# Kernel optimization log

Measured on AMD Instinct MI355X. Metric: run time of the kernel, lower is better.

## Reference

```python
import math
import jax, jax.numpy as jnp
import numpy as np

NH, HD, CHUNK, PAST, FUT = 12, 128, 128, 127, 0  # heads, head_dim, chunk, left-1, right
CTX = CHUNK + PAST + FUT                          # 255
Q_SCALE = HD ** (-0.5) / math.log(2.0)
K_SCALE = math.log1p(math.e) / math.log(2.0)
SOFTCAP = 50.0


def setup_inputs() -> dict:
    key = jax.random.key(0)
    ks = jax.random.split(key, 8)
    B, S, H = 4, 4096, NH * HD
    return {
        "hidden_states": jax.random.normal(ks[0], (B, S, H), jnp.float32),
        "position_embeddings": jax.random.normal(ks[1], (CTX, H), jnp.float32),
        "Wq": jax.random.normal(ks[2], (H, H), jnp.float32) * 0.02,
        "Wk": jax.random.normal(ks[3], (H, H), jnp.float32) * 0.02,
        "Wv": jax.random.normal(ks[4], (H, H), jnp.float32) * 0.02,
        "Wrel": jax.random.normal(ks[5], (H, H), jnp.float32) * 0.02,
        "Wpost": jax.random.normal(ks[6], (H, H), jnp.float32) * 0.02,
        "per_dim_scale": jax.random.normal(ks[7], (HD,), jnp.float32) * 0.1,
    }


def reference(hidden_states, position_embeddings, Wq, Wk, Wv, Wrel, Wpost, per_dim_scale):
    B, S, H = hidden_states.shape
    # projections -> [B, S, nh, hd]; per-dim softplus scaling on queries (Gemma audio)
    q = (hidden_states @ Wq.T).reshape(B, S, NH, HD)
    q = q * (Q_SCALE * jax.nn.softplus(per_dim_scale))
    k = (hidden_states @ Wk.T).reshape(B, S, NH, HD) * K_SCALE
    v = (hidden_states @ Wv.T).reshape(B, S, NH, HD)

    NB = (S + CHUNK - 1) // CHUNK
    pad = NB * CHUNK - S
    q_blk = jnp.pad(q, ((0, 0), (0, pad), (0, 0), (0, 0))).reshape(B, NB, CHUNK, NH, HD)

    def extract_block_context(x):
        # pad [PAST] front, [FUT + CHUNK - 1] back; overlapping windows of CTX, stride CHUNK
        xp = jnp.pad(x, ((0, 0), (PAST, FUT + CHUNK - 1), (0, 0), (0, 0)))
        idx = jnp.arange(NB)[:, None] * CHUNK + jnp.arange(CTX)[None, :]  # [NB, CTX]
        return xp[:, idx]  # [B, NB, CTX, nh, hd]

    k_ctx = extract_block_context(k)
    v_ctx = extract_block_context(v)

    # content scores: [B, nh, NB, CHUNK, CTX]
    ac = jnp.einsum('bnchd,bnxhd->bhncx', q_blk, k_ctx)

    # relative-position scores with Transformer-XL style rel_shift
    rel_k = (position_embeddings @ Wrel.T).reshape(-1, NH, HD)  # [P, nh, hd]
    bd = jnp.einsum('bnchd,phd->bhncp', q_blk, rel_k)            # [B, nh, NB, CHUNK, P]
    P = bd.shape[-1]
    bd = jnp.pad(bd, ((0, 0), (0, 0), (0, 0), (0, 0), (0, CTX + 1 - P)))
    bd = bd.reshape(B, NH, NB, CHUNK * (CTX + 1))[..., : CHUNK * CTX]
    bd = bd.reshape(B, NH, NB, CHUNK, CTX)

    logits = SOFTCAP * jnp.tanh((ac + bd) / SOFTCAP)  # softcap
    w = jax.nn.softmax(logits, axis=-1)

    out = jnp.einsum('bhncx,bnxhd->bnchd', w, v_ctx)  # [B, NB, CHUNK, nh, hd]
    out = out.reshape(B, NB * CHUNK, NH * HD)[:, :S]
    return out @ Wpost.T
```

## Files before the change

kernel.cpp:

```cpp
#include <hip/hip_runtime.h>
#include <hip/hip_bf16.h>
#include <math.h>


#define NH_    12
#define HD_    128
#define H_     1536
#define B_     4
#define S_     4096
#define CHUNK_ 128
#define CTX_   255
#define NB_CH  32
#define QKW_   3072
#define BSTR_  4352

typedef unsigned short u16;
typedef short bf16x8 __attribute__((ext_vector_type(8)));
typedef float f32x4 __attribute__((ext_vector_type(4)));

static constexpr float Q_SCALE_F = (float)(0.08838834764831845 / 0.6931471805599453);
static constexpr float K_SCALE_F = (float)(1.3132616875182228 / 0.6931471805599453);

__device__ __forceinline__ u16 f2bf(float f) {
    __hip_bfloat16 h = __float2bfloat16(f);
    return __builtin_bit_cast(u16, h);
}
__device__ __forceinline__ float bf2f(u16 u) {
    unsigned int t = ((unsigned int)u) << 16;
    return __builtin_bit_cast(float, t);
}
__device__ __forceinline__ float fast_tanh(float t) {
    float u = __expf(-2.f * fabsf(t));
    float r = (1.f - u) / (1.f + u);
    return (t < 0.f) ? -r : r;
}

__device__ __forceinline__ void gload_lds16(const u16* src_global, u16* dst_lds) {
    __builtin_amdgcn_global_load_lds(
        (const __attribute__((address_space(1))) unsigned int*)src_global,
        (__attribute__((address_space(3))) unsigned int*)dst_lds,
        16, 0, 0);
}

__global__ __launch_bounds__(256)
void conv_bf16(const float* __restrict__ src, long long base,
               u16* __restrict__ dst, long long n,
               long long zero_below, long long zero_from,
               int mode, const float* __restrict__ pds, int ncols)
{
    long long i = ((long long)blockIdx.x * 256 + threadIdx.x) * 4;
    if (i >= n) return;
    float4 v = make_float4(0.f, 0.f, 0.f, 0.f);
    if (i >= zero_below && i < zero_from)
        v = *(const float4*)(src + base + i);
    float s = 1.f;
    if (mode == 1) {
        int row = (int)(i / ncols);
        float x = pds[row & 127];
        float sp = (x > 20.f) ? x : log1pf(__expf(x));
        s = Q_SCALE_F * sp;
    } else if (mode == 2) {
        s = K_SCALE_F;
    }
    ushort4 o = make_ushort4(f2bf(v.x * s), f2bf(v.y * s), f2bf(v.z * s), f2bf(v.w * s));
    *(ushort4*)(dst + i) = o;
}

__global__ __launch_bounds__(256)
void conv_hs(const float* __restrict__ src, long long src_row0,
             u16* __restrict__ dst, long long nelem)
{
    long long i = ((long long)blockIdx.x * 256 + threadIdx.x) * 4;
    if (i >= nelem) return;
    const int row = (int)(i / H_);
    const int col = (int)(i - (long long)row * H_);
    const int b = row / BSTR_;
    const int local = row - b * BSTR_;
    float4 v = make_float4(0.f, 0.f, 0.f, 0.f);
    if (local >= 128 && local < 128 + S_) {
        const long long srow = src_row0 + (long long)b * S_ + local - 128;
        v = *(const float4*)(src + srow * H_ + col);
    }
    ushort4 o = make_ushort4(f2bf(v.x), f2bf(v.y), f2bf(v.z), f2bf(v.w));
    *(ushort4*)(dst + i) = o;
}

#define STAGE(kt, bufc) do {                                                   \
    const int _ko = (kt) << 5;                                                 \
    gload_lds16(srcA[0] + _ko, lds + (bufc) * 4096 + pbase[0]);                \
    gload_lds16(srcA[1] + _ko, lds + (bufc) * 4096 + pbase[1]);                \
    gload_lds16(srcB[0] + _ko, lds + 16384 + (bufc) * 4096 + pbase[0]);        \
    gload_lds16(srcB[1] + _ko, lds + 16384 + (bufc) * 4096 + pbase[1]);        \
} while (0)

#define READF(afX, bfX, b) do {                                                \
    _Pragma("unroll")                                                          \
    for (int m = 0; m < 4; ++m)                                                \
        afX[m] = *(const bf16x8*)&lds[(b) * 4096 + (wr + m * 16 + lr) * 32 + sw8]; \
    _Pragma("unroll")                                                          \
    for (int n = 0; n < 4; ++n)                                                \
        bfX[n] = *(const bf16x8*)&lds[16384 + (b) * 4096 + (wc + n * 16 + lr) * 32 + sw8]; \
} while (0)

#define MFMA16(afX, bfX) do {                                                  \
    __builtin_amdgcn_s_setprio(1);                                             \
    _Pragma("unroll")                                                          \
    for (int m = 0; m < 4; ++m)                                                \
        _Pragma("unroll")                                                      \
        for (int n = 0; n < 4; ++n)                                            \
            acc[m][n] = __builtin_amdgcn_mfma_f32_16x16x32_bf16(afX[m], bfX[n], acc[m][n], 0, 0, 0); \
    __builtin_amdgcn_s_setprio(0);                                             \
} while (0)

#define ITER(t, b, afC, bfC, afN, bfN) do {                                    \
    if ((t) + 2 < nk) {                                                        \
        STAGE((t) + 2, ((b) + 2) & 3);                                         \
        asm volatile("s_waitcnt vmcnt(4)" ::: "memory");                       \
    } else {                                                                   \
        asm volatile("s_waitcnt vmcnt(0)" ::: "memory");                       \
    }                                                                          \
    __builtin_amdgcn_s_barrier();                                              \
    if ((t) + 1 < nk) READF(afN, bfN, ((b) + 1) & 3);                          \
    MFMA16(afC, bfC);                                                          \
} while (0)

__global__ __launch_bounds__(256)
void gemm_bt(const u16* __restrict__ A, const u16* __restrict__ B,
             u16* __restrict__ Cp, int M, int N, int K, int ldc)
{
    __shared__ __align__(16) u16 lds[32768];

    const int tid = threadIdx.x;
    const int w = tid >> 6, l = tid & 63;
    const int lr = l & 15, lg = l >> 4;
    const int bm = blockIdx.y * 128, bn = blockIdx.x * 128;
    const int wr = (w >> 1) * 64, wc = (w & 1) * 64;
    const int sw8 = (lg ^ ((lr >> 1) & 3)) * 8;

    const u16* srcA[2];
    const u16* srcB[2];
    int pbase[2];
#pragma unroll
    for (int c = 0; c < 2; ++c) {
        const int p = (w * 2 + c) * 64 + l;
        const int row = p >> 2;
        const int s_log = (p & 3) ^ ((row >> 1) & 3);
        pbase[c] = p * 8;
        srcA[c] = A + (size_t)(bm + row) * K + s_log * 8;
        srcB[c] = B + (size_t)(bn + row) * K + s_log * 8;
    }

    f32x4 acc[4][4];
#pragma unroll
    for (int m = 0; m < 4; ++m)
#pragma unroll
        for (int n = 0; n < 4; ++n) acc[m][n] = (f32x4){0.f, 0.f, 0.f, 0.f};

    const int nk = K >> 5;
    bf16x8 af0[4], bf0[4], af1[4], bf1[4];

    STAGE(0, 0);
    STAGE(1, 1);
    asm volatile("s_waitcnt vmcnt(4)" ::: "memory");
    __builtin_amdgcn_s_barrier();
    READF(af0, bf0, 0);

    for (int t0 = 0; t0 < nk; t0 += 4) {
        ITER(t0 + 0, 0, af0, bf0, af1, bf1);
        ITER(t0 + 1, 1, af1, bf1, af0, bf0);
        ITER(t0 + 2, 2, af0, bf0, af1, bf1);
        ITER(t0 + 3, 3, af1, bf1, af0, bf0);
    }

#pragma unroll
    for (int h = 0; h < 2; ++h) {
        if (wr == h * 64) {
#pragma unroll
            for (int m = 0; m < 4; ++m)
#pragma unroll
                for (int n = 0; n < 4; ++n)
#pragma unroll
                    for (int r = 0; r < 4; ++r)
                        lds[(m * 16 + lg * 4 + r) * 136 + wc + n * 16 + lr] =
                            f2bf(acc[m][n][r]);
        }
        __syncthreads();
#pragma unroll
        for (int it = 0; it < 4; ++it) {
            const int sid = it * 256 + tid;
            const int row = sid >> 4, sl = sid & 15;
            int4 val = *(const int4*)&lds[row * 136 + sl * 8];
            *(int4*)(Cp + (size_t)(bm + h * 64 + row) * ldc + bn + sl * 8) = val;
        }
        __syncthreads();
    }
}

#define STG2(kt, bufc) do {                                                    \
    const int _ko = (kt) << 5;                                                 \
    gload_lds16(srcA[0] + _ko, lds + (bufc) * 16384 + pbase[0]);               \
    gload_lds16(srcA[1] + _ko, lds + (bufc) * 16384 + pbase[1]);               \
    gload_lds16(srcB[0] + _ko, lds + (bufc) * 16384 + 8192 + pbase[0]);        \
    gload_lds16(srcB[1] + _ko, lds + (bufc) * 16384 + 8192 + pbase[1]);        \
} while (0)

#define IT3(t, b) do {                                                         \
    if ((t) + 3 < nk) {                                                        \
        STG2((t) + 3, ((b) + 3) & 3);                                          \
        asm volatile("s_waitcnt vmcnt(12)" ::: "memory");                      \
    } else if ((t) + 3 == nk) {                                                \
        asm volatile("s_waitcnt vmcnt(8)" ::: "memory");                       \
    } else if ((t) + 2 == nk) {                                                \
        asm volatile("s_waitcnt vmcnt(4)" ::: "memory");                       \
    } else {                                                                   \
        asm volatile("s_waitcnt vmcnt(0)" ::: "memory");                       \
    }                                                                          \
    __builtin_amdgcn_s_barrier();                                              \
    bf16x8 af[8], bfr[4];                                                      \
    _Pragma("unroll")                                                          \
    for (int m = 0; m < 8; ++m)                                                \
        af[m] = *(const bf16x8*)&lds[(b) * 16384 + (mbase + m * 16 + lr) * 32 + sw8]; \
    _Pragma("unroll")                                                          \
    for (int n = 0; n < 4; ++n)                                                \
        bfr[n] = *(const bf16x8*)&lds[(b) * 16384 + 8192 + (nbase + n * 16 + lr) * 32 + sw8]; \
    __builtin_amdgcn_s_setprio(1);                                             \
    _Pragma("unroll")                                                          \
    for (int m = 0; m < 8; ++m)                                                \
        _Pragma("unroll")                                                      \
        for (int n = 0; n < 4; ++n)                                            \
            acc[m][n] = __builtin_amdgcn_mfma_f32_16x16x32_bf16(af[m], bfr[n], acc[m][n], 0, 0, 0); \
    __builtin_amdgcn_s_setprio(0);                                             \
} while (0)

template<int OUTB>
__device__ __forceinline__
void gemm256_body(const u16* __restrict__ A, const u16* __restrict__ B,
                  void* __restrict__ Cp, int N, int K, int ldc,
                  int bx, int by, u16* lds)
{
    (void)N;
    const int tid = threadIdx.x;
    const int w = tid >> 6, l = tid & 63;
    const int lr = l & 15, lg = l >> 4;
    const int wrow = w >> 2, wcol = w & 3;
    const int bm = by * 256, bn = bx * 256;
    const int mbase = wrow * 128;
    const int nbase = wcol * 64;
    const int sw8 = (lg ^ ((lr >> 1) & 3)) * 8;

    const u16* srcA[2];
    const u16* srcB[2];
    int pbase[2];
#pragma unroll
    for (int c = 0; c < 2; ++c) {
        const int p = c * 512 + tid;
        const int row = p >> 2;
        const int s_log = (p & 3) ^ ((row >> 1) & 3);
        pbase[c] = p * 8;
        srcA[c] = A + (size_t)(bm + row) * K + s_log * 8;
        srcB[c] = B + (size_t)(bn + row) * K + s_log * 8;
    }

    f32x4 acc[8][4];
#pragma unroll
    for (int m = 0; m < 8; ++m)
#pragma unroll
        for (int n = 0; n < 4; ++n) acc[m][n] = (f32x4){0.f, 0.f, 0.f, 0.f};

    const int nk = K >> 5;
    STG2(0, 0);
    STG2(1, 1);
    STG2(2, 2);
    for (int t0 = 0; t0 < nk; t0 += 4) {
        IT3(t0 + 0, 0);
        IT3(t0 + 1, 1);
        IT3(t0 + 2, 2);
        IT3(t0 + 3, 3);
    }

    __syncthreads();

    if (OUTB) {
#pragma unroll
        for (int h = 0; h < 2; ++h) {
            if (wrow == h) {
#pragma unroll
                for (int m = 0; m < 8; ++m)
#pragma unroll
                    for (int n = 0; n < 4; ++n)
#pragma unroll
                        for (int r = 0; r < 4; ++r)
                            lds[(m * 16 + lg * 4 + r) * 264 + nbase + n * 16 + lr] =
                                f2bf(acc[m][n][r]);
            }
            __syncthreads();
#pragma unroll
            for (int it = 0; it < 8; ++it) {
                const int sid = it * 512 + tid;
                const int row = sid >> 5, sl = sid & 31;
                int4 val = *(const int4*)&lds[row * 264 + sl * 8];
                *(int4*)((u16*)Cp + (size_t)(bm + h * 128 + row) * ldc + bn + sl * 8) = val;
            }
            __syncthreads();
        }
    } else {
#pragma unroll
        for (int m = 0; m < 8; ++m)
#pragma unroll
            for (int n = 0; n < 4; ++n)
#pragma unroll
                for (int r = 0; r < 4; ++r) {
                    const int row = bm + mbase + m * 16 + lg * 4 + r;
                    const int col = bn + nbase + n * 16 + lr;
                    ((float*)Cp)[(size_t)row * ldc + col] = acc[m][n][r];
                }
    }
}

__global__ __launch_bounds__(512, 2)
void gemm256_dual(const u16* __restrict__ A1, const u16* __restrict__ B1,
                  void* __restrict__ C1, int N1, int K1, int ldc1, int nx1,
                  const u16* __restrict__ A2, const u16* __restrict__ B2,
                  void* __restrict__ C2, int N2, int K2, int ldc2, int nx2,
                  int nqk)
{
    __shared__ __align__(16) u16 lds[65536];
    const int flat = blockIdx.x;
    if (flat < nqk) {
        gemm256_body<1>(A1, B1, C1, N1, K1, ldc1, flat % nx1, flat / nx1, lds);
    } else {
        const int local = flat - nqk;
        gemm256_body<1>(A2, B2, C2, N2, K2, ldc2, local % nx2, local / nx2, lds);
    }
}

template<int OUTB>
__global__ __launch_bounds__(512, 2)
void gemm256(const u16* __restrict__ A, const u16* __restrict__ B,
             void* __restrict__ Cp, int N, int K, int ldc)
{
    __shared__ __align__(16) u16 lds[65536];
    gemm256_body<OUTB>(A, B, Cp, N, K, ldc, blockIdx.x, blockIdx.y, lds);
}

__global__ __launch_bounds__(512)
void attn_mfma(const u16* __restrict__ qk, const u16* __restrict__ vT,
               const u16* __restrict__ relk, u16* __restrict__ attn_out,
               int vld)
{
    __shared__ __align__(16) u16 kv_s[256 * 128];
    __shared__ __align__(16) u16 g_s[128 * 264];

    const int ln = blockIdx.x, h = blockIdx.y, bz = blockIdx.z;
    const int tid = threadIdx.x;
    const int w = tid >> 6, l = tid & 63;
    const int lr = l & 15, lg = l >> 4;
    const size_t qbase = (size_t)bz * BSTR_;
    const size_t qrow0 = qbase + (size_t)(ln + 1) * 128;

    bf16x8 qa[4];
    {
        const u16* qp = qk + (qrow0 + w * 16 + lr) * QKW_ + h * HD_ + lg * 8;
#pragma unroll
        for (int kk = 0; kk < 4; ++kk) qa[kk] = *(const bf16x8*)(qp + kk * 32);
    }

#pragma unroll
    for (int it = 0; it < 8; ++it) {
        const int p = it * 512 + tid;
        const int row = p >> 4;
        const int s_log = (p & 15) ^ (row & 15);
        gload_lds16(relk + (size_t)row * H_ + h * HD_ + s_log * 8, kv_s + p * 8);
    }
    __syncthreads();

    f32x4 sacc[16];
#pragma unroll
    for (int n = 0; n < 16; ++n) sacc[n] = (f32x4){0.f, 0.f, 0.f, 0.f};
#pragma unroll
    for (int n = 0; n < 16; ++n)
#pragma unroll
        for (int kk = 0; kk < 4; ++kk) {
            int row = n * 16 + lr;
            int sl = kk * 4 + lg;
            bf16x8 bfrag = *(const bf16x8*)&kv_s[row * 128 + ((sl ^ (row & 15)) << 3)];
            sacc[n] = __builtin_amdgcn_mfma_f32_16x16x32_bf16(qa[kk], bfrag, sacc[n], 0, 0, 0);
        }

    const int c = w * 16 + lg * 4;
#pragma unroll
    for (int n = 0; n < 16; ++n)
#pragma unroll
        for (int r = 0; r < 4; ++r)
            g_s[(c + r) * 264 + n * 16 + lr] = f2bf(sacc[n][r]);
    __syncthreads();

#pragma unroll
    for (int it = 0; it < 8; ++it) {
        const int p = it * 512 + tid;
        const int row = p >> 4;
        const int s_log = (p & 15) ^ (row & 15);
        gload_lds16(qk + (qbase + (size_t)(ln * 128 + 1 + row)) * QKW_ + 1536 + h * HD_ + s_log * 8,
                    kv_s + p * 8);
    }
    __syncthreads();

#pragma unroll
    for (int n = 0; n < 16; ++n) sacc[n] = (f32x4){0.f, 0.f, 0.f, 0.f};
#pragma unroll
    for (int n = 0; n < 16; ++n)
#pragma unroll
        for (int kk = 0; kk < 4; ++kk) {
            int row = n * 16 + lr;
            int sl = kk * 4 + lg;
            bf16x8 bfrag = *(const bf16x8*)&kv_s[row * 128 + ((sl ^ (row & 15)) << 3)];
            sacc[n] = __builtin_amdgcn_mfma_f32_16x16x32_bf16(qa[kk], bfrag, sacc[n], 0, 0, 0);
        }

#pragma unroll
    for (int n = 0; n < 16; ++n)
#pragma unroll
        for (int r = 0; r < 4; ++r) {
            int cc = c + r;
            int x = n * 16 + lr;
            float val;
            if (x == 255) {
                val = -1e30f;
            } else {
                int dx = x - cc;
                u16 bdu = (dx >= 0) ? g_s[cc * 264 + dx]
                                    : g_s[(cc - 1) * 264 + dx + 256];
                float t = (sacc[n][r] + bf2f(bdu)) * (1.f / 50.f);
                val = 50.f * fast_tanh(t);
            }
            sacc[n][r] = val;
        }

#pragma unroll
    for (int r = 0; r < 4; ++r) {
        float m = -1e30f;
#pragma unroll
        for (int n = 0; n < 16; ++n) m = fmaxf(m, sacc[n][r]);
#pragma unroll
        for (int off = 1; off < 16; off <<= 1) m = fmaxf(m, __shfl_xor(m, off, 16));
        float s = 0.f;
#pragma unroll
        for (int n = 0; n < 16; ++n) {
            float e = __expf(sacc[n][r] - m);
            sacc[n][r] = e;
            s += e;
        }
#pragma unroll
        for (int off = 1; off < 16; off <<= 1) s += __shfl_xor(s, off, 16);
        float inv = 1.f / s;
#pragma unroll
        for (int n = 0; n < 16; ++n) sacc[n][r] *= inv;
    }
    __syncthreads();

#pragma unroll
    for (int n = 0; n < 16; ++n)
#pragma unroll
        for (int r = 0; r < 4; ++r)
            g_s[(c + r) * 264 + n * 16 + lr] = f2bf(sacc[n][r]);

#pragma unroll
    for (int it = 0; it < 8; ++it) {
        const int p = it * 512 + tid;
        const int d = p >> 5;
        const int s_log = (p & 31) ^ (d & 15);
        gload_lds16(vT + (size_t)(h * HD_ + d) * vld + qbase + ln * 128 + 1 + s_log * 8,
                    kv_s + p * 8);
    }
    __syncthreads();

    f32x4 oacc[8];
#pragma unroll
    for (int n = 0; n < 8; ++n) oacc[n] = (f32x4){0.f, 0.f, 0.f, 0.f};
#pragma unroll
    for (int kk = 0; kk < 8; ++kk) {
        int prow = w * 16 + lr;
        bf16x8 pa = *(const bf16x8*)&g_s[prow * 264 + kk * 32 + lg * 8];
#pragma unroll
        for (int n = 0; n < 8; ++n) {
            int d = n * 16 + lr;
            int sl = kk * 4 + lg;
            bf16x8 vb = *(const bf16x8*)&kv_s[d * 256 + ((sl ^ (d & 15)) << 3)];
            oacc[n] = __builtin_amdgcn_mfma_f32_16x16x32_bf16(pa, vb, oacc[n], 0, 0, 0);
        }
    }

    __syncthreads();
#pragma unroll
    for (int n = 0; n < 8; ++n)
#pragma unroll
        for (int r = 0; r < 4; ++r)
            kv_s[(c + r) * 136 + n * 16 + lr] = f2bf(oacc[n][r]);
    __syncthreads();
#pragma unroll
    for (int it = 0; it < 4; ++it) {
        const int sid = it * 512 + tid;
        const int row = sid >> 4, sl = sid & 15;
        int4 val = *(const int4*)&kv_s[row * 136 + sl * 8];
        *(int4*)(attn_out + ((size_t)bz * S_ + (size_t)(ln * 128 + row)) * H_ + h * HD_ + sl * 8) = val;
    }
}

extern "C" void kernel_launch(void* const* d_in, const int* in_sizes, int n_in,
                              void* d_out, int out_size, void* d_ws, size_t ws_size,
                              hipStream_t stream)
{
    (void)in_sizes; (void)n_in; (void)out_size;

    const float* hs    = (const float*)d_in[0];
    const float* pos   = (const float*)d_in[1];
    const float* Wq    = (const float*)d_in[2];
    const float* Wk    = (const float*)d_in[3];
    const float* Wv    = (const float*)d_in[4];
    const float* Wrel  = (const float*)d_in[5];
    const float* Wpost = (const float*)d_in[6];
    const float* pds   = (const float*)d_in[7];
    float* out = (float*)d_out;

    const long long WW = (long long)H_ * H_;
    const long long POSN = 256LL * H_;
    const long long fixed_elems = 5 * WW + 2 * POSN;

    int NB = 0;
    const int cand[3] = {4, 2, 1};
    for (int ci = 0; ci < 3; ++ci) {
        const int nb = cand[ci];
        const long long R = (long long)nb * BSTR_;
        const long long seg = R * (H_ + QKW_ + H_) + (long long)nb * S_ * H_;
        if ((fixed_elems + seg) * 2 <= (long long)ws_size) { NB = nb; break; }
    }
    if (NB == 0) return;

    const long long R = (long long)NB * BSTR_;
    const int vld = (int)R;

    u16* wqkb   = (u16*)d_ws;
    u16* wvb    = wqkb + 2 * WW;
    u16* wpostb = wvb + WW;
    u16* wrelb  = wpostb + WW;
    u16* posb   = wrelb + WW;
    u16* relkb  = posb + POSN;
    u16* hsb    = relkb + POSN;
    u16* qkb    = hsb + R * H_;
    u16* vTb    = qkb + R * QKW_;
    u16* attb   = vTb + (long long)H_ * R;

    dim3 blk(256);
    const long long BIG = 1LL << 60;

    conv_bf16<<<dim3(WW / 1024), blk, 0, stream>>>(Wq, 0, wqkb,        WW, 0, BIG, 1, pds, H_);
    conv_bf16<<<dim3(WW / 1024), blk, 0, stream>>>(Wk, 0, wqkb + WW,   WW, 0, BIG, 2, nullptr, H_);
    conv_bf16<<<dim3(WW / 1024), blk, 0, stream>>>(Wv, 0, wvb,         WW, 0, BIG, 0, nullptr, H_);
    conv_bf16<<<dim3(WW / 1024), blk, 0, stream>>>(Wpost, 0, wpostb,   WW, 0, BIG, 0, nullptr, H_);
    conv_bf16<<<dim3(WW / 1024), blk, 0, stream>>>(Wrel, 0, wrelb,     WW, 0, BIG, 0, nullptr, H_);
    conv_bf16<<<dim3(POSN / 1024), blk, 0, stream>>>(pos, 0, posb, POSN, 0, 255LL * H_, 0, nullptr, H_);

    gemm_bt<<<dim3(H_ / 128, 2), blk, 0, stream>>>(posb, wrelb, relkb, 256, H_, H_, H_);

    const long long hn = R * H_;
    const int nx1 = QKW_ / 256;
    const int nqk = nx1 * (int)(R / 256);
    const int nx2 = (int)(R / 256);
    const int nvt = nx2 * (H_ / 256);

    for (int s = 0; s < B_ / NB; ++s) {
        const long long row0 = (long long)s * NB * S_;

        conv_hs<<<dim3((unsigned)(hn / 1024)), blk, 0, stream>>>(hs, row0, hsb, hn);

        gemm256_dual<<<dim3((unsigned)(nqk + nvt)), dim3(512), 0, stream>>>(
            hsb, wqkb, qkb, QKW_, H_, QKW_, nx1,
            wvb, hsb, vTb, (int)R, H_, vld, nx2,
            nqk);

        attn_mfma<<<dim3(NB_CH, NH_, NB), dim3(512), 0, stream>>>(
            qkb, vTb, relkb, attb, vld);

        gemm256<0><<<dim3(H_ / 256, (unsigned)((long long)NB * S_ / 256)), dim3(512), 0, stream>>>(
            attb, wpostb, out + row0 * H_, H_, H_, H_);
    }
}
```

Measured before the change: 541.1 us.

## Prefetch K and V tiles into registers to overlap global loads with MFMA

Replaces the direct global-to-LDS loads for the K and V tiles with register prefetches issued one stage early. K is loaded while the rel-pos GEMM runs and V while the content GEMM runs, then each is written to swizzled LDS. Full __syncthreads are replaced by manual waitcnt plus s_barrier, so the global-load latency hides behind compute. The cost is 8 extra int4 registers per thread, which may lower occupancy, and a reliance on hand-counted vmcnt values for correctness.

```diff
diff --git a/kernel.cpp b/kernel.cpp
--- a/kernel.cpp
+++ b/kernel.cpp
@@ -364,6 +364,7 @@
 #pragma unroll
         for (int kk = 0; kk < 4; ++kk) qa[kk] = *(const bf16x8*)(qp + kk * 32);
     }
+    asm volatile("" ::: "memory");
 
 #pragma unroll
     for (int it = 0; it < 8; ++it) {
@@ -372,7 +373,20 @@
         const int s_log = (p & 15) ^ (row & 15);
         gload_lds16(relk + (size_t)row * H_ + h * HD_ + s_log * 8, kv_s + p * 8);
     }
-    __syncthreads();
+    asm volatile("" ::: "memory");
+
+    int4 kvreg[8];
+#pragma unroll
+    for (int it = 0; it < 8; ++it) {
+        const int p = it * 512 + tid;
+        const int row = p >> 4;
+        const int sl = p & 15;
+        kvreg[it] = *(const int4*)(qk + (qbase + (size_t)(ln * 128 + 1 + row)) * QKW_
+                                   + 1536 + h * HD_ + sl * 8);
+    }
+
+    asm volatile("s_waitcnt vmcnt(8)" ::: "memory");
+    __builtin_amdgcn_s_barrier();
 
     f32x4 sacc[16];
 #pragma unroll
@@ -399,11 +413,21 @@
     for (int it = 0; it < 8; ++it) {
         const int p = it * 512 + tid;
         const int row = p >> 4;
-        const int s_log = (p & 15) ^ (row & 15);
-        gload_lds16(qk + (qbase + (size_t)(ln * 128 + 1 + row)) * QKW_ + 1536 + h * HD_ + s_log * 8,
-                    kv_s + p * 8);
-    }
-    __syncthreads();
+        const int sl = p & 15;
+        *(int4*)&kv_s[row * 128 + (((sl ^ (row & 15)) << 3))] = kvreg[it];
+    }
+
+#pragma unroll
+    for (int it = 0; it < 8; ++it) {
+        const int p = it * 512 + tid;
+        const int d = p >> 5;
+        const int sl = p & 31;
+        kvreg[it] = *(const int4*)(vT + (size_t)(h * HD_ + d) * vld
+                                   + qbase + ln * 128 + 1 + sl * 8);
+    }
+
+    asm volatile("s_waitcnt lgkmcnt(0)" ::: "memory");
+    __builtin_amdgcn_s_barrier();
 
 #pragma unroll
     for (int n = 0; n < 16; ++n) sacc[n] = (f32x4){0.f, 0.f, 0.f, 0.f};
@@ -468,11 +492,11 @@
     for (int it = 0; it < 8; ++it) {
         const int p = it * 512 + tid;
         const int d = p >> 5;
-        const int s_log = (p & 31) ^ (d & 15);
-        gload_lds16(vT + (size_t)(h * HD_ + d) * vld + qbase + ln * 128 + 1 + s_log * 8,
-                    kv_s + p * 8);
-    }
-    __syncthreads();
+        const int sl = p & 31;
+        *(int4*)&kv_s[d * 256 + (((sl ^ (d & 15)) << 3))] = kvreg[it];
+    }
+    asm volatile("s_waitcnt lgkmcnt(0)" ::: "memory");
+    __builtin_amdgcn_s_barrier();
 
     f32x4 oacc[8];
 #pragma unroll
```

Result: slower. 595.3 us (+10.0%).

## Double-buffer attention LDS to overlap K and V loads with MFMA compute

Applied to the files above, without the earlier changes.

Splits the attention kernel's shared memory into two equal buffers. The K-context load is now issued alongside the rel-pos load, and the V load is issued before the softcap/softmax phase. Partial vmcnt waits and raw s_barrier calls replace __syncthreads so global-to-LDS transfers overlap the relative-position and content MFMA work. This adds more LDS per block and hand-managed waitcnt ordering, which is fragile if the load count or ordering assumptions are wrong.

```diff
diff --git a/kernel.cpp b/kernel.cpp
--- a/kernel.cpp
+++ b/kernel.cpp
@@ -348,8 +348,8 @@
                const u16* __restrict__ relk, u16* __restrict__ attn_out,
                int vld)
 {
-    __shared__ __align__(16) u16 kv_s[256 * 128];
-    __shared__ __align__(16) u16 g_s[128 * 264];
+    __shared__ __align__(16) u16 bufA[33792];
+    __shared__ __align__(16) u16 bufB[33792];
 
     const int ln = blockIdx.x, h = blockIdx.y, bz = blockIdx.z;
     const int tid = threadIdx.x;
@@ -364,36 +364,16 @@
 #pragma unroll
         for (int kk = 0; kk < 4; ++kk) qa[kk] = *(const bf16x8*)(qp + kk * 32);
     }
+    asm volatile("" ::: "memory");
 
 #pragma unroll
     for (int it = 0; it < 8; ++it) {
         const int p = it * 512 + tid;
         const int row = p >> 4;
         const int s_log = (p & 15) ^ (row & 15);
-        gload_lds16(relk + (size_t)row * H_ + h * HD_ + s_log * 8, kv_s + p * 8);
-    }
-    __syncthreads();
-
-    f32x4 sacc[16];
-#pragma unroll
-    for (int n = 0; n < 16; ++n) sacc[n] = (f32x4){0.f, 0.f, 0.f, 0.f};
-#pragma unroll
-    for (int n = 0; n < 16; ++n)
-#pragma unroll
-        for (int kk = 0; kk < 4; ++kk) {
-            int row = n * 16 + lr;
-            int sl = kk * 4 + lg;
-            bf16x8 bfrag = *(const bf16x8*)&kv_s[row * 128 + ((sl ^ (row & 15)) << 3)];
-            sacc[n] = __builtin_amdgcn_mfma_f32_16x16x32_bf16(qa[kk], bfrag, sacc[n], 0, 0, 0);
-        }
-
-    const int c = w * 16 + lg * 4;
-#pragma unroll
-    for (int n = 0; n < 16; ++n)
-#pragma unroll
-        for (int r = 0; r < 4; ++r)
-            g_s[(c + r) * 264 + n * 16 + lr] = f2bf(sacc[n][r]);
-    __syncthreads();
+        gload_lds16(relk + (size_t)row * H_ + h * HD_ + s_log * 8, bufB + p * 8);
+    }
+    asm volatile("" ::: "memory");
 
 #pragma unroll
     for (int it = 0; it < 8; ++it) {
@@ -401,10 +381,12 @@
         const int row = p >> 4;
         const int s_log = (p & 15) ^ (row & 15);
         gload_lds16(qk + (qbase + (size_t)(ln * 128 + 1 + row)) * QKW_ + 1536 + h * HD_ + s_log * 8,
-                    kv_s + p * 8);
-    }
-    __syncthreads();
-
+                    bufA + p * 8);
+    }
+    asm volatile("s_waitcnt vmcnt(8)" ::: "memory");
+    __builtin_amdgcn_s_barrier();
+
+    f32x4 sacc[16];
 #pragma unroll
     for (int n = 0; n < 16; ++n) sacc[n] = (f32x4){0.f, 0.f, 0.f, 0.f};
 #pragma unroll
@@ -413,9 +395,44 @@
         for (int kk = 0; kk < 4; ++kk) {
             int row = n * 16 + lr;
             int sl = kk * 4 + lg;
-            bf16x8 bfrag = *(const bf16x8*)&kv_s[row * 128 + ((sl ^ (row & 15)) << 3)];
+            bf16x8 bfrag = *(const bf16x8*)&bufB[row * 128 + ((sl ^ (row & 15)) << 3)];
             sacc[n] = __builtin_amdgcn_mfma_f32_16x16x32_bf16(qa[kk], bfrag, sacc[n], 0, 0, 0);
         }
+
+    asm volatile("s_waitcnt vmcnt(0)" ::: "memory");
+    __builtin_amdgcn_s_barrier();
+
+    const int c = w * 16 + lg * 4;
+#pragma unroll
+    for (int n = 0; n < 16; ++n)
+#pragma unroll
+        for (int r = 0; r < 4; ++r)
+            bufB[(c + r) * 264 + n * 16 + lr] = f2bf(sacc[n][r]);
+    asm volatile("s_waitcnt lgkmcnt(0)" ::: "memory");
+    __builtin_amdgcn_s_barrier();
+
+#pragma unroll
+    for (int n = 0; n < 16; ++n) sacc[n] = (f32x4){0.f, 0.f, 0.f, 0.f};
+#pragma unroll
+    for (int n = 0; n < 16; ++n)
+#pragma unroll
+        for (int kk = 0; kk < 4; ++kk) {
+            int row = n * 16 + lr;
+            int sl = kk * 4 + lg;
+            bf16x8 bfrag = *(const bf16x8*)&bufA[row * 128 + ((sl ^ (row & 15)) << 3)];
+            sacc[n] = __builtin_amdgcn_mfma_f32_16x16x32_bf16(qa[kk], bfrag, sacc[n], 0, 0, 0);
+        }
+
+    __builtin_amdgcn_s_barrier();
+
+#pragma unroll
+    for (int it = 0; it < 8; ++it) {
+        const int p = it * 512 + tid;
+        const int d = p >> 5;
+        const int s_log = (p & 31) ^ (d & 15);
+        gload_lds16(vT + (size_t)(h * HD_ + d) * vld + qbase + ln * 128 + 1 + s_log * 8,
+                    bufA + p * 8);
+    }
 
 #pragma unroll
     for (int n = 0; n < 16; ++n)
@@ -428,8 +445,8 @@
                 val = -1e30f;
             } else {
                 int dx = x - cc;
-                u16 bdu = (dx >= 0) ? g_s[cc * 264 + dx]
-                                    : g_s[(cc - 1) * 264 + dx + 256];
+                u16 bdu = (dx >= 0) ? bufB[cc * 264 + dx]
+                                    : bufB[(cc - 1) * 264 + dx + 256];
                 float t = (sacc[n][r] + bf2f(bdu)) * (1.f / 50.f);
                 val = 50.f * fast_tanh(t);
             }
@@ -456,23 +473,15 @@
 #pragma unroll
         for (int n = 0; n < 16; ++n) sacc[n][r] *= inv;
     }
-    __syncthreads();
+    __builtin_amdgcn_s_barrier();
 
 #pragma unroll
     for (int n = 0; n < 16; ++n)
 #pragma unroll
         for (int r = 0; r < 4; ++r)
-            g_s[(c + r) * 264 + n * 16 + lr] = f2bf(sacc[n][r]);
-
-#pragma unroll
-    for (int it = 0; it < 8; ++it) {
-        const int p = it * 512 + tid;
-        const int d = p >> 5;
-        const int s_log = (p & 31) ^ (d & 15);
-        gload_lds16(vT + (size_t)(h * HD_ + d) * vld + qbase + ln * 128 + 1 + s_log * 8,
-                    kv_s + p * 8);
-    }
-    __syncthreads();
+            bufB[(c + r) * 264 + n * 16 + lr] = f2bf(sacc[n][r]);
+    asm volatile("s_waitcnt vmcnt(0) lgkmcnt(0)" ::: "memory");
+    __builtin_amdgcn_s_barrier();
 
     f32x4 oacc[8];
 #pragma unroll
@@ -480,12 +489,12 @@
 #pragma unroll
     for (int kk = 0; kk < 8; ++kk) {
         int prow = w * 16 + lr;
-        bf16x8 pa = *(const bf16x8*)&g_s[prow * 264 + kk * 32 + lg * 8];
+        bf16x8 pa = *(const bf16x8*)&bufB[prow * 264 + kk * 32 + lg * 8];
 #pragma unroll
         for (int n = 0; n < 8; ++n) {
             int d = n * 16 + lr;
             int sl = kk * 4 + lg;
-            bf16x8 vb = *(const bf16x8*)&kv_s[d * 256 + ((sl ^ (d & 15)) << 3)];
+            bf16x8 vb = *(const bf16x8*)&bufA[d * 256 + ((sl ^ (d & 15)) << 3)];
             oacc[n] = __builtin_amdgcn_mfma_f32_16x16x32_bf16(pa, vb, oacc[n], 0, 0, 0);
         }
     }
@@ -495,13 +504,13 @@
     for (int n = 0; n < 8; ++n)
 #pragma unroll
         for (int r = 0; r < 4; ++r)
-            kv_s[(c + r) * 136 + n * 16 + lr] = f2bf(oacc[n][r]);
+            bufA[(c + r) * 136 + n * 16 + lr] = f2bf(oacc[n][r]);
     __syncthreads();
 #pragma unroll
     for (int it = 0; it < 4; ++it) {
         const int sid = it * 512 + tid;
         const int row = sid >> 4, sl = sid & 15;
-        int4 val = *(const int4*)&kv_s[row * 136 + sl * 8];
+        int4 val = *(const int4*)&bufA[row * 136 + sl * 8];
         *(int4*)(attn_out + ((size_t)bz * S_ + (size_t)(ln * 128 + row)) * H_ + h * HD_ + sl * 8) = val;
     }
 }
```

After: 539.5 us. Within noise of the previous version (-0.3%).
